# Kernel optimization log

Measured on AMD Instinct MI355X. Metric: run time of the kernel, lower is better.

The kernel has to match this reference:

```python
import jax, jax.numpy as jnp
import numpy as np
from jax import lax

B, C, T = 8, 512, 2048
TEMP = 0.07
EPS = 1e-12


def setup_inputs() -> dict:
    key = jax.random.key(0)
    k1, k2, k3, k4 = jax.random.split(key, 4)
    x = jax.random.normal(k1, (B, C, T), dtype=jnp.float32)
    w_qkv = jax.random.normal(k2, (3 * C, C, 1), dtype=jnp.float32) * (1.0 / np.sqrt(C))
    w_dw = jax.random.normal(k3, (3 * C, 1, 3), dtype=jnp.float32) * (1.0 / np.sqrt(3))
    w_proj = jax.random.normal(k4, (C, C, 1), dtype=jnp.float32) * (1.0 / np.sqrt(C))
    return {"x": x, "w_qkv": w_qkv, "w_dw": w_dw, "w_proj": w_proj}


def _l2norm_ch(a):
    # F.normalize(a, dim=1): divide by L2 norm over channel dim, clamped at eps
    n = jnp.sqrt(jnp.sum(a * a, axis=1, keepdims=True))
    return a / jnp.maximum(n, EPS)


def reference(x, w_qkv, w_dw, w_proj):
    # 1x1 conv: [B,C,T] x [3C,C] -> [B,3C,T]
    qkv = jnp.einsum('bct,oc->bot', x, w_qkv[:, :, 0])
    # depthwise conv, kernel 3, padding 1, groups = 3C
    qkv = lax.conv_general_dilated(
        qkv, w_dw, window_strides=(1,), padding=[(1, 1)],
        dimension_numbers=('NCH', 'OIH', 'NCH'), feature_group_count=3 * C)
    q, k, v = jnp.split(qkv, 3, axis=1)  # each [B,C,T]
    q = _l2norm_ch(q)
    k = _l2norm_ch(k)
    # attn over tokens: [B,T,T]
    attn = jax.nn.softmax(jnp.einsum('bct,bcs->bts', q, k) / TEMP, axis=-1)
    out = jnp.einsum('bts,bcs->bct', attn, v)  # [B,C,T]
    return jnp.einsum('bct,oc->bot', out, w_proj[:, :, 0])
```

## Files before the change

kernel.cpp:

```cpp
#include <hip/hip_runtime.h>
#include <math.h>

static constexpr int B_ = 8, C_ = 512, T_ = 2048, C3_ = 1536;
static constexpr float INV_TEMP = 1.0f / 0.07f;

typedef __attribute__((ext_vector_type(8))) short short8;
typedef __attribute__((ext_vector_type(4))) float floatx4;

__device__ __forceinline__ float b2f(unsigned short u) {
  union { unsigned int i; float f; } v; v.i = ((unsigned int)u) << 16; return v.f;
}
__device__ __forceinline__ unsigned short f2b(float f) {
  union { float f; unsigned int i; } v; v.f = f;
  const unsigned int x = v.i;
  return (unsigned short)((x + 0x7FFFu + ((x >> 16) & 1u)) >> 16);
}
__device__ __forceinline__ void gld16(const unsigned short* g, unsigned short* l) {
  __builtin_amdgcn_global_load_lds(
      (const __attribute__((address_space(1))) void*)g,
      (__attribute__((address_space(3))) void*)l, 16, 0, 0);
}

template<bool OUT_BF16, int MODE>
__global__ __launch_bounds__(256)
void gemm_tn(const unsigned short* __restrict__ A, const unsigned short* __restrict__ B,
             void* __restrict__ Cout, int K, int lda, int ldb, int ldc,
             long long sA, long long sB, long long sC,
             const float* __restrict__ rs, const float* __restrict__ cs,
             float* __restrict__ denom, int rcStride, float scale)
{
  constexpr int NL = 4;

  const int bz = blockIdx.z;
  A += (long long)bz * sA;
  B += (long long)bz * sB;
  if (MODE == 2) { rs += (long long)bz * rcStride; cs += (long long)bz * rcStride;
                   denom += (long long)bz * rcStride; }
  if (MODE == 3) { rs += (long long)bz * rcStride; }
  const int m0 = blockIdx.y * 128, n0 = blockIdx.x * 128;
  const int tid = threadIdx.x;
  const int w = tid >> 6, lane = tid & 63;
  const int wm = (w >> 1) * 64, wn = (w & 1) * 64;
  const int rl = lane & 15, qd = lane >> 4;

  __shared__ __align__(16) unsigned short As[3][128 * 32];
  __shared__ __align__(16) unsigned short Bs[3][128 * 32];

  const int sr = lane >> 2, sg = lane & 3;
  const int ml0 = 32 * w + sr, ml1 = ml0 + 16;
  const int q0 = sg ^ ((ml0 >> 1) & 3), q1 = sg ^ ((ml1 >> 1) & 3);
  const unsigned short* gA0 = A + (long long)(m0 + ml0) * lda + q0 * 8;
  const unsigned short* gA1 = A + (long long)(m0 + ml1) * lda + q1 * 8;
  const unsigned short* gB0 = B + (long long)(n0 + ml0) * ldb + q0 * 8;
  const unsigned short* gB1 = B + (long long)(n0 + ml1) * ldb + q1 * 8;

  int aoff[4], boff[4];
  #pragma unroll
  for (int i = 0; i < 4; ++i) {
    const int mr = wm + i * 16 + rl;
    aoff[i] = mr * 32 + ((qd ^ ((mr >> 1) & 3)) * 8);
    const int nr = wn + i * 16 + rl;
    boff[i] = nr * 32 + ((qd ^ ((nr >> 1) & 3)) * 8);
  }

  floatx4 acc[4][4];
  #pragma unroll
  for (int i = 0; i < 4; ++i)
    #pragma unroll
    for (int j = 0; j < 4; ++j) acc[i][j] = 0.0f;

  auto stage = [&](int t, int bf) {
    const int ko = t * 32;
    gld16(gA0 + ko, As[bf] + (32 * w) * 32);
    gld16(gA1 + ko, As[bf] + (32 * w + 16) * 32);
    gld16(gB0 + ko, Bs[bf] + (32 * w) * 32);
    gld16(gB1 + ko, Bs[bf] + (32 * w + 16) * 32);
  };
  auto compute = [&](int bf) {
    short8 fa[4], fb[4];
    #pragma unroll
    for (int i = 0; i < 4; ++i) fa[i] = *(const short8*)(As[bf] + aoff[i]);
    #pragma unroll
    for (int j = 0; j < 4; ++j) fb[j] = *(const short8*)(Bs[bf] + boff[j]);
    #pragma unroll
    for (int i = 0; i < 4; ++i)
      #pragma unroll
      for (int j = 0; j < 4; ++j)
        acc[i][j] = __builtin_amdgcn_mfma_f32_16x16x32_bf16(fa[i], fb[j], acc[i][j], 0, 0, 0);
  };

  const int niter = K >> 5;
  stage(0, 0);
  stage(1, 1);
  int buf = 0;
  for (int i = 0; i < niter - 1; ++i) {
    asm volatile("s_waitcnt vmcnt(%0)\n\ts_barrier" :: "i"(NL) : "memory");
    if (i + 2 < niter) {
      int nb = buf + 2; if (nb >= 3) nb -= 3;
      stage(i + 2, nb);
    }
    compute(buf);
    if (++buf == 3) buf = 0;
  }
  asm volatile("s_waitcnt vmcnt(0)\n\ts_barrier" ::: "memory");
  compute(buf);

  #pragma unroll
  for (int i = 0; i < 4; ++i) {
    #pragma unroll
    for (int r = 0; r < 4; ++r) {
      const int row = m0 + wm + i * 16 + qd * 4 + r;
      float rowf = 0.f;
      if (MODE == 2) rowf = rs[row] * scale;
      if (MODE == 3) rowf = 1.0f / rs[row];
      float rsum = 0.f;
      #pragma unroll
      for (int j = 0; j < 4; ++j) {
        const int col = n0 + wn + j * 16 + rl;
        float v = acc[i][j][r];
        if (MODE == 2) {
          const float s = v * rowf * cs[col];
          const unsigned short pb = f2b(__expf(s - scale));
          rsum += b2f(pb);
          ((unsigned short*)Cout)[(long long)bz * sC + (long long)row * ldc + col] = pb;
          continue;
        }
        if (MODE == 3) v *= rowf;
        const long long idx = (long long)bz * sC + (long long)row * ldc + col;
        if (OUT_BF16) ((unsigned short*)Cout)[idx] = f2b(v);
        else          ((float*)Cout)[idx] = v;
      }
      if (MODE == 2) {
        #pragma unroll
        for (int m = 1; m < 16; m <<= 1) rsum += __shfl_xor(rsum, m);
        if (rl == 0) atomicAdd(denom + row, rsum);
      }
    }
  }
}

__global__ __launch_bounds__(256)
void zero_f(float* __restrict__ p, int n)
{
  const int i = blockIdx.x * 256 + threadIdx.x;
  if (i < n) p[i] = 0.f;
}

__global__ __launch_bounds__(256)
void conv_xT(const float* __restrict__ x, unsigned short* __restrict__ xT)
{
  const int b = blockIdx.z, t0 = blockIdx.x * 32, c0 = blockIdx.y * 32;
  const int tx = threadIdx.x & 31, ty = threadIdx.x >> 5;
  __shared__ float tile[32][33];
  const float* src = x + (long long)b * C_ * T_;
  #pragma unroll
  for (int r = 0; r < 4; ++r)
    tile[ty + 8 * r][tx] = src[(long long)(c0 + ty + 8 * r) * T_ + t0 + tx];
  __syncthreads();
  unsigned short* dst = xT + (long long)b * T_ * C_;
  #pragma unroll
  for (int r = 0; r < 4; ++r)
    dst[(long long)(t0 + ty + 8 * r) * C_ + c0 + tx] = f2b(tile[tx][ty + 8 * r]);
}

__global__ __launch_bounds__(256)
void conv_bf(const float* __restrict__ in, unsigned short* __restrict__ out, int n)
{
  const int i = blockIdx.x * 256 + threadIdx.x;
  if (i < n) out[i] = f2b(in[i]);
}

__global__ __launch_bounds__(256)
void dw_v(const unsigned short* __restrict__ qkv, const float* __restrict__ wdw,
          unsigned short* __restrict__ vout)
{
  const long long idx = (long long)blockIdx.x * 256 + threadIdx.x;
  const int t = (int)(idx % T_);
  const long long rem = idx / T_;
  const int c = (int)(rem % C_), b = (int)(rem / C_);
  const unsigned short* src = qkv + ((long long)(b * C3_ + 2 * C_ + c)) * T_;
  const float* wp = wdw + (2 * C_ + c) * 3;
  const float xm = (t > 0)      ? b2f(src[t - 1]) : 0.f;
  const float x0 = b2f(src[t]);
  const float xp = (t < T_ - 1) ? b2f(src[t + 1]) : 0.f;
  vout[(long long)(b * C_ + c) * T_ + t] = f2b(fmaf(wp[0], xm, fmaf(wp[1], x0, wp[2] * xp)));
}

__global__ __launch_bounds__(256)
void dw_qk_t(const unsigned short* __restrict__ qkv, const float* __restrict__ wdw,
             unsigned short* __restrict__ qT, unsigned short* __restrict__ kT)
{
  const int bz = blockIdx.z, b = bz >> 1, p = bz & 1;
  const int t0 = blockIdx.x * 32, c0 = blockIdx.y * 32;
  const int tx = threadIdx.x & 31, ty = threadIdx.x >> 5;
  __shared__ float tin[32][34];
  __shared__ float tout[32][33];
  const int chb = b * C3_ + p * C_;
  #pragma unroll
  for (int r = 0; r < 4; ++r) {
    const int cy = ty + 8 * r;
    const unsigned short* src = qkv + (long long)(chb + c0 + cy) * T_;
    int t = t0 - 1 + tx;
    tin[cy][tx] = (t >= 0 && t < T_) ? b2f(src[t]) : 0.f;
    if (tx < 2) {
      const int t2 = t0 + 31 + tx;
      tin[cy][32 + tx] = (t2 < T_) ? b2f(src[t2]) : 0.f;
    }
  }
  __syncthreads();
  #pragma unroll
  for (int r = 0; r < 4; ++r) {
    const int cy = ty + 8 * r;
    const float* wp = wdw + (long long)(p * C_ + c0 + cy) * 3;
    tout[tx][cy] = fmaf(wp[0], tin[cy][tx], fmaf(wp[1], tin[cy][tx + 1], wp[2] * tin[cy][tx + 2]));
  }
  __syncthreads();
  unsigned short* dst = (p == 0 ? qT : kT) + (long long)b * T_ * C_;
  #pragma unroll
  for (int r = 0; r < 4; ++r)
    dst[(long long)(t0 + ty + 8 * r) * C_ + c0 + tx] = f2b(tout[ty + 8 * r][tx]);
}

__global__ __launch_bounds__(256)
void norms_k(const unsigned short* __restrict__ qT, const unsigned short* __restrict__ kT,
             float* __restrict__ inv_nq, float* __restrict__ inv_nk)
{
  const int wave = threadIdx.x >> 6, lane = threadIdx.x & 63;
  const long long row = (long long)blockIdx.x * 4 + wave;
  const unsigned short* src = (blockIdx.y == 0 ? qT : kT) + row * C_ + lane * 8;
  const uint4 u = *(const uint4*)src;
  float ss = 0.f;
  const unsigned int uu[4] = {u.x, u.y, u.z, u.w};
  #pragma unroll
  for (int i = 0; i < 4; ++i) {
    const float lo = b2f(uu[i] & 0xFFFF), hi = b2f(uu[i] >> 16);
    ss = fmaf(lo, lo, ss); ss = fmaf(hi, hi, ss);
  }
  #pragma unroll
  for (int m = 32; m; m >>= 1) ss += __shfl_xor(ss, m);
  if (lane == 0)
    (blockIdx.y == 0 ? inv_nq : inv_nk)[row] = 1.f / fmaxf(sqrtf(ss), 1e-12f);
}

extern "C" void kernel_launch(void* const* d_in, const int* in_sizes, int n_in,
                              void* d_out, int out_size, void* d_ws, size_t ws_size,
                              hipStream_t stream)
{
  const float* x      = (const float*)d_in[0];
  const float* w_qkv  = (const float*)d_in[1];
  const float* w_dw   = (const float*)d_in[2];
  const float* w_proj = (const float*)d_in[3];
  float* out = (float*)d_out;

  char* base = (char*)d_ws;
  unsigned short* xT      = (unsigned short*)base;
  unsigned short* wqkv_bf = (unsigned short*)(base + 16777216);
  unsigned short* av_t    = (unsigned short*)base;
  char* p = base + 67108864;
  unsigned short* qT = (unsigned short*)p; p += 16777216;
  unsigned short* kT = (unsigned short*)p; p += 16777216;
  unsigned short* vb = (unsigned short*)p; p += 16777216;
  unsigned short* attn   = (unsigned short*)p;
  unsigned short* qkv_bf = (unsigned short*)p;
  p += 67108864;
  unsigned short* wproj_bf = (unsigned short*)p; p += 524288;
  float* inv_nq = (float*)p; p += 65536;
  float* inv_nk = (float*)p; p += 65536;
  float* denom  = (float*)p;

  const long long TC = (long long)T_ * C_, TT = (long long)T_ * T_;

  conv_xT<<<dim3(T_ / 32, C_ / 32, B_), 256, 0, stream>>>(x, xT);
  conv_bf<<<(C3_ * C_) / 256, 256, 0, stream>>>(w_qkv, wqkv_bf, C3_ * C_);
  conv_bf<<<(C_ * C_) / 256, 256, 0, stream>>>(w_proj, wproj_bf, C_ * C_);
  zero_f<<<(B_ * T_) / 256, 256, 0, stream>>>(denom, B_ * T_);

  gemm_tn<true, 0><<<dim3(16, 12, B_), 256, 0, stream>>>(
      wqkv_bf, xT, qkv_bf, C_, C_, C_, T_,
      0LL, TC, (long long)C3_ * T_, nullptr, nullptr, nullptr, 0, 1.f);

  dw_v<<<(int)(((long long)B_ * C_ * T_) / 256), 256, 0, stream>>>(qkv_bf, w_dw, vb);
  dw_qk_t<<<dim3(T_ / 32, C_ / 32, B_ * 2), 256, 0, stream>>>(qkv_bf, w_dw, qT, kT);

  norms_k<<<dim3((B_ * T_) / 4, 2), 256, 0, stream>>>(qT, kT, inv_nq, inv_nk);

  gemm_tn<true, 2><<<dim3(16, 16, B_), 256, 0, stream>>>(
      qT, kT, attn, C_, C_, C_, T_,
      TC, TC, TT, inv_nq, inv_nk, denom, T_, INV_TEMP);

  gemm_tn<true, 3><<<dim3(4, 16, B_), 256, 0, stream>>>(
      attn, vb, av_t, T_, T_, T_, C_,
      TT, (long long)C_ * T_, TC, denom, nullptr, nullptr, T_, 1.f);

  gemm_tn<false, 0><<<dim3(16, 4, B_), 256, 0, stream>>>(
      wproj_bf, av_t, out, C_, C_, C_, T_,
      0LL, TC, (long long)C_ * T_, nullptr, nullptr, nullptr, 0, 1.f);
}
```

Before: 335.3 us.

## Replace 128x128 GEMM with 256x256 eight-wave ping-pong pipelined kernel

Rewrites the shared GEMM kernel to use 256x256 output tiles with 512 threads, K-step 64, and 128KB of dynamic LDS. A fine-grained schedule of barriers and s_setprio interleaves LDS fragment reads, async global-to-LDS loads and MFMA blocks. The aim is more data reuse per tile and more overlap of loads with compute. The trade-offs are fewer blocks for the small GEMMs (for example 128 blocks for the AV and projection GEMMs), heavy LDS use and many barriers.

```diff
diff --git a/kernel.cpp b/kernel.cpp
--- a/kernel.cpp
+++ b/kernel.cpp
@@ -21,15 +21,21 @@
       (__attribute__((address_space(3))) void*)l, 16, 0, 0);
 }
 
+#define FENCE  asm volatile("" ::: "memory")
+#define BAR()  do { FENCE; __builtin_amdgcn_s_barrier(); FENCE; } while (0)
+#define LGKM0  asm volatile("s_waitcnt lgkmcnt(0)" ::: "memory")
+#define VMC4   asm volatile("s_waitcnt vmcnt(4)" ::: "memory")
+#define VMC0   asm volatile("s_waitcnt vmcnt(0)" ::: "memory")
+
 template<bool OUT_BF16, int MODE>
-__global__ __launch_bounds__(256)
-void gemm_tn(const unsigned short* __restrict__ A, const unsigned short* __restrict__ B,
+__global__ __launch_bounds__(512, 2)
+void gemm256(const unsigned short* __restrict__ A, const unsigned short* __restrict__ B,
              void* __restrict__ Cout, int K, int lda, int ldb, int ldc,
              long long sA, long long sB, long long sC,
              const float* __restrict__ rs, const float* __restrict__ cs,
              float* __restrict__ denom, int rcStride, float scale)
 {
-  constexpr int NL = 4;
+  extern __shared__ unsigned short S[];
 
   const int bz = blockIdx.z;
   A += (long long)bz * sA;
@@ -37,76 +43,125 @@
   if (MODE == 2) { rs += (long long)bz * rcStride; cs += (long long)bz * rcStride;
                    denom += (long long)bz * rcStride; }
   if (MODE == 3) { rs += (long long)bz * rcStride; }
-  const int m0 = blockIdx.y * 128, n0 = blockIdx.x * 128;
+  const int m0 = blockIdx.y * 256, n0 = blockIdx.x * 256;
   const int tid = threadIdx.x;
   const int w = tid >> 6, lane = tid & 63;
-  const int wm = (w >> 1) * 64, wn = (w & 1) * 64;
   const int rl = lane & 15, qd = lane >> 4;
-
-  __shared__ __align__(16) unsigned short As[3][128 * 32];
-  __shared__ __align__(16) unsigned short Bs[3][128 * 32];
-
-  const int sr = lane >> 2, sg = lane & 3;
-  const int ml0 = 32 * w + sr, ml1 = ml0 + 16;
-  const int q0 = sg ^ ((ml0 >> 1) & 3), q1 = sg ^ ((ml1 >> 1) & 3);
-  const unsigned short* gA0 = A + (long long)(m0 + ml0) * lda + q0 * 8;
-  const unsigned short* gA1 = A + (long long)(m0 + ml1) * lda + q1 * 8;
-  const unsigned short* gB0 = B + (long long)(n0 + ml0) * ldb + q0 * 8;
-  const unsigned short* gB1 = B + (long long)(n0 + ml1) * ldb + q1 * 8;
-
-  int aoff[4], boff[4];
-  #pragma unroll
-  for (int i = 0; i < 4; ++i) {
-    const int mr = wm + i * 16 + rl;
-    aoff[i] = mr * 32 + ((qd ^ ((mr >> 1) & 3)) * 8);
-    const int nr = wn + i * 16 + rl;
-    boff[i] = nr * 32 + ((qd ^ ((nr >> 1) & 3)) * 8);
-  }
-
-  floatx4 acc[4][4];
-  #pragma unroll
-  for (int i = 0; i < 4; ++i)
+  const int wm = (w >> 2) * 128, wn = (w & 3) * 64;
+
+  const int lr = lane >> 3;
+  const int lg = ((lane & 7) ^ lr) * 8;
+  const unsigned short* gA = A + (long long)(m0 + w * 8 + lr) * lda + lg;
+  const unsigned short* gB = B + (long long)(n0 + w * 8 + lr) * ldb + lg;
+
+  const int g0 = (qd ^ (rl & 7)) * 8;
+  const int g1 = ((4 + qd) ^ (rl & 7)) * 8;
+  const int aBase = (wm + rl) * 64, bBase = (wn + rl) * 64;
+
+  floatx4 acc[8][4];
+  #pragma unroll
+  for (int i = 0; i < 8; ++i)
     #pragma unroll
     for (int j = 0; j < 4; ++j) acc[i][j] = 0.0f;
 
-  auto stage = [&](int t, int bf) {
-    const int ko = t * 32;
-    gld16(gA0 + ko, As[bf] + (32 * w) * 32);
-    gld16(gA1 + ko, As[bf] + (32 * w + 16) * 32);
-    gld16(gB0 + ko, Bs[bf] + (32 * w) * 32);
-    gld16(gB1 + ko, Bs[bf] + (32 * w + 16) * 32);
-  };
-  auto compute = [&](int bf) {
-    short8 fa[4], fb[4];
-    #pragma unroll
-    for (int i = 0; i < 4; ++i) fa[i] = *(const short8*)(As[bf] + aoff[i]);
-    #pragma unroll
-    for (int j = 0; j < 4; ++j) fb[j] = *(const short8*)(Bs[bf] + boff[j]);
+  auto stA = [&](int buf, int h, int kt) {
+    unsigned short* d = S + buf * 32768 + h * 8192 + w * 512;
+    const unsigned short* s = gA + (long long)(h * 128) * lda + kt * 64;
+    gld16(s, d);
+    gld16(s + (long long)64 * lda, d + 4096);
+  };
+  auto stB = [&](int buf, int h, int kt) {
+    unsigned short* d = S + buf * 32768 + 16384 + h * 8192 + w * 512;
+    const unsigned short* s = gB + (long long)(h * 128) * ldb + kt * 64;
+    gld16(s, d);
+    gld16(s + (long long)64 * ldb, d + 4096);
+  };
+
+  short8 fa[4][2], fl[2][2], fr[2][2];
+  auto rdA = [&](int buf, int ih) {
+    const unsigned short* p = S + buf * 32768 + aBase + ih * 4096;
+    #pragma unroll
+    for (int i = 0; i < 4; ++i) {
+      fa[i][0] = *(const short8*)(p + i * 1024 + g0);
+      fa[i][1] = *(const short8*)(p + i * 1024 + g1);
+    }
+  };
+  auto rdB = [&](short8 (&fb)[2][2], int buf, int jh) {
+    const unsigned short* p = S + buf * 32768 + 16384 + bBase + jh * 2048;
+    #pragma unroll
+    for (int j = 0; j < 2; ++j) {
+      fb[j][0] = *(const short8*)(p + j * 1024 + g0);
+      fb[j][1] = *(const short8*)(p + j * 1024 + g1);
+    }
+  };
+  auto mm = [&](short8 (&fb)[2][2], int ih, int jh) {
     #pragma unroll
     for (int i = 0; i < 4; ++i)
       #pragma unroll
-      for (int j = 0; j < 4; ++j)
-        acc[i][j] = __builtin_amdgcn_mfma_f32_16x16x32_bf16(fa[i], fb[j], acc[i][j], 0, 0, 0);
-  };
-
-  const int niter = K >> 5;
-  stage(0, 0);
-  stage(1, 1);
-  int buf = 0;
-  for (int i = 0; i < niter - 1; ++i) {
-    asm volatile("s_waitcnt vmcnt(%0)\n\ts_barrier" :: "i"(NL) : "memory");
-    if (i + 2 < niter) {
-      int nb = buf + 2; if (nb >= 3) nb -= 3;
-      stage(i + 2, nb);
-    }
-    compute(buf);
-    if (++buf == 3) buf = 0;
-  }
-  asm volatile("s_waitcnt vmcnt(0)\n\ts_barrier" ::: "memory");
-  compute(buf);
-
-  #pragma unroll
-  for (int i = 0; i < 4; ++i) {
+      for (int j = 0; j < 2; ++j) {
+        floatx4& a = acc[ih * 4 + i][jh * 2 + j];
+        a = __builtin_amdgcn_mfma_f32_16x16x32_bf16(fa[i][0], fb[j][0], a, 0, 0, 0);
+        a = __builtin_amdgcn_mfma_f32_16x16x32_bf16(fa[i][1], fb[j][1], a, 0, 0, 0);
+      }
+  };
+
+  auto iter = [&](int kt, bool st2, bool st3, bool tail) {
+    rdA(0, 0); rdB(fl, 0, 0);
+    stA(1, 0, kt + 1);
+    BAR(); LGKM0;
+    __builtin_amdgcn_s_setprio(1); mm(fl, 0, 0); __builtin_amdgcn_s_setprio(0);
+    BAR();
+    rdB(fr, 0, 1);
+    stA(1, 1, kt + 1);
+    BAR(); LGKM0;
+    __builtin_amdgcn_s_setprio(1); mm(fr, 0, 1); __builtin_amdgcn_s_setprio(0);
+    BAR();
+    rdA(0, 1);
+    if (st2) stB(0, 0, kt + 2);
+    BAR(); LGKM0;
+    __builtin_amdgcn_s_setprio(1); mm(fl, 1, 0); __builtin_amdgcn_s_setprio(0);
+    BAR();
+    if (st2) stB(0, 1, kt + 2);
+    if (tail) { VMC0; } else { VMC4; }
+    BAR();
+    __builtin_amdgcn_s_setprio(1); mm(fr, 1, 1); __builtin_amdgcn_s_setprio(0);
+    BAR();
+    rdA(1, 0); rdB(fl, 1, 0);
+    if (st2) stA(0, 0, kt + 2);
+    BAR(); LGKM0;
+    __builtin_amdgcn_s_setprio(1); mm(fl, 0, 0); __builtin_amdgcn_s_setprio(0);
+    BAR();
+    rdB(fr, 1, 1);
+    if (st2) stA(0, 1, kt + 2);
+    BAR(); LGKM0;
+    __builtin_amdgcn_s_setprio(1); mm(fr, 0, 1); __builtin_amdgcn_s_setprio(0);
+    BAR();
+    rdA(1, 1);
+    if (st3) stB(1, 0, kt + 3);
+    BAR(); LGKM0;
+    __builtin_amdgcn_s_setprio(1); mm(fl, 1, 0); __builtin_amdgcn_s_setprio(0);
+    BAR();
+    if (st3) stB(1, 1, kt + 3);
+    if (!tail) { VMC4; }
+    BAR();
+    __builtin_amdgcn_s_setprio(1); mm(fr, 1, 1); __builtin_amdgcn_s_setprio(0);
+    BAR();
+  };
+
+  const int niter = K >> 7;
+  stB(0, 0, 0); stB(0, 1, 0); stA(0, 0, 0); stA(0, 1, 0);
+  stB(1, 0, 1); stB(1, 1, 1);
+  VMC4; BAR();
+  for (int i = 0; i < niter - 1; ++i) iter(2 * i, true, true, false);
+  iter(2 * (niter - 1), false, false, true);
+
+  float cf4[4];
+  if (MODE == 2) {
+    #pragma unroll
+    for (int j = 0; j < 4; ++j) cf4[j] = cs[n0 + wn + j * 16 + rl];
+  }
+  #pragma unroll
+  for (int i = 0; i < 8; ++i) {
     #pragma unroll
     for (int r = 0; r < 4; ++r) {
       const int row = m0 + wm + i * 16 + qd * 4 + r;
@@ -119,7 +174,7 @@
         const int col = n0 + wn + j * 16 + rl;
         float v = acc[i][j][r];
         if (MODE == 2) {
-          const float s = v * rowf * cs[col];
+          const float s = v * rowf * cf4[j];
           const unsigned short pb = f2b(__expf(s - scale));
           rsum += b2f(pb);
           ((unsigned short*)Cout)[(long long)bz * sC + (long long)row * ldc + col] = pb;
@@ -252,6 +307,19 @@
   const float* w_proj = (const float*)d_in[3];
   float* out = (float*)d_out;
 
+  static int attr_done = 0;
+  if (!attr_done) {
+    hipFuncSetAttribute((const void*)&gemm256<true, 0>,
+                        hipFuncAttributeMaxDynamicSharedMemorySize, 131072);
+    hipFuncSetAttribute((const void*)&gemm256<true, 2>,
+                        hipFuncAttributeMaxDynamicSharedMemorySize, 131072);
+    hipFuncSetAttribute((const void*)&gemm256<true, 3>,
+                        hipFuncAttributeMaxDynamicSharedMemorySize, 131072);
+    hipFuncSetAttribute((const void*)&gemm256<false, 0>,
+                        hipFuncAttributeMaxDynamicSharedMemorySize, 131072);
+    attr_done = 1;
+  }
+
   char* base = (char*)d_ws;
   unsigned short* xT      = (unsigned short*)base;
   unsigned short* wqkv_bf = (unsigned short*)(base + 16777216);
@@ -275,7 +343,7 @@
   conv_bf<<<(C_ * C_) / 256, 256, 0, stream>>>(w_proj, wproj_bf, C_ * C_);
   zero_f<<<(B_ * T_) / 256, 256, 0, stream>>>(denom, B_ * T_);
 
-  gemm_tn<true, 0><<<dim3(16, 12, B_), 256, 0, stream>>>(
+  gemm256<true, 0><<<dim3(8, 6, B_), 512, 131072, stream>>>(
       wqkv_bf, xT, qkv_bf, C_, C_, C_, T_,
       0LL, TC, (long long)C3_ * T_, nullptr, nullptr, nullptr, 0, 1.f);
 
@@ -284,15 +352,15 @@
 
   norms_k<<<dim3((B_ * T_) / 4, 2), 256, 0, stream>>>(qT, kT, inv_nq, inv_nk);
 
-  gemm_tn<true, 2><<<dim3(16, 16, B_), 256, 0, stream>>>(
+  gemm256<true, 2><<<dim3(8, 8, B_), 512, 131072, stream>>>(
       qT, kT, attn, C_, C_, C_, T_,
       TC, TC, TT, inv_nq, inv_nk, denom, T_, INV_TEMP);
 
-  gemm_tn<true, 3><<<dim3(4, 16, B_), 256, 0, stream>>>(
+  gemm256<true, 3><<<dim3(2, 8, B_), 512, 131072, stream>>>(
       attn, vb, av_t, T_, T_, T_, C_,
       TT, (long long)C_ * T_, TC, denom, nullptr, nullptr, T_, 1.f);
 
-  gemm_tn<false, 0><<<dim3(16, 4, B_), 256, 0, stream>>>(
+  gemm256<false, 0><<<dim3(8, 2, B_), 512, 131072, stream>>>(
       wproj_bf, av_t, out, C_, C_, C_, T_,
       0LL, TC, (long long)C_ * T_, nullptr, nullptr, nullptr, 0, 1.f);
 }
```

New measurement: 340.9 us. No clear change (+1.7%).

## Fuse depthwise conv with norms and use 256x256-tile QK GEMM

Applied to the files above, without the earlier changes.

Merges the v and q/k depthwise-conv kernels into one launch. The sum-of-squares norm reduction moves into the conv epilogue through atomics, followed by a small finalize kernel, which removes the separate norms pass that re-read qT/kT. The QK^T softmax-numerator GEMM is switched to a new 1024-thread kernel with 256x256 tiles and triple-buffered dynamic LDS, to raise data reuse. The risks are lower occupancy from the 96KB LDS blocks, the cost of the atomic contention, and only 512 blocks to spread across the CUs.

```diff
diff --git a/kernel.cpp b/kernel.cpp
--- a/kernel.cpp
+++ b/kernel.cpp
@@ -139,11 +139,125 @@
   }
 }
 
+template<bool OUT_BF16, int MODE>
+__global__ __launch_bounds__(1024)
+void gemm_tn1024(const unsigned short* __restrict__ A, const unsigned short* __restrict__ B,
+                 void* __restrict__ Cout, int K, int lda, int ldb, int ldc,
+                 long long sA, long long sB, long long sC,
+                 const float* __restrict__ rs, const float* __restrict__ cs,
+                 float* __restrict__ denom, int rcStride, float scale)
+{
+  extern __shared__ unsigned short S[];
+
+  const int bz = blockIdx.z;
+  A += (long long)bz * sA;
+  B += (long long)bz * sB;
+  if (MODE == 2) { rs += (long long)bz * rcStride; cs += (long long)bz * rcStride;
+                   denom += (long long)bz * rcStride; }
+  if (MODE == 3) { rs += (long long)bz * rcStride; }
+  const int m0 = blockIdx.y * 256, n0 = blockIdx.x * 256;
+  const int tid = threadIdx.x;
+  const int w = tid >> 6, lane = tid & 63;
+  const int wm = (w >> 2) * 64, wn = (w & 3) * 64;
+  const int rl = lane & 15, qd = lane >> 4;
+
+  const int srow = w * 16 + (lane >> 2), sg = lane & 3;
+  const int qa = sg ^ ((srow >> 1) & 3);
+  const unsigned short* gA = A + (long long)(m0 + srow) * lda + qa * 8;
+  const unsigned short* gB = B + (long long)(n0 + srow) * ldb + qa * 8;
+
+  const int ar = wm + rl, br = wn + rl;
+  const int aoff0 = ar * 32 + ((qd ^ ((ar >> 1) & 3)) * 8);
+  const int boff0 = br * 32 + ((qd ^ ((br >> 1) & 3)) * 8);
+
+  floatx4 acc[4][4];
+  #pragma unroll
+  for (int i = 0; i < 4; ++i)
+    #pragma unroll
+    for (int j = 0; j < 4; ++j) acc[i][j] = 0.0f;
+
+  auto stage = [&](int t, int bf) {
+    const int ko = t * 32;
+    gld16(gA + ko, S + bf * 16384 + w * 512);
+    gld16(gB + ko, S + bf * 16384 + 8192 + w * 512);
+  };
+  auto compute = [&](int bf) {
+    short8 fa[4], fb[4];
+    const unsigned short* pA = S + bf * 16384 + aoff0;
+    const unsigned short* pB = S + bf * 16384 + 8192 + boff0;
+    #pragma unroll
+    for (int i = 0; i < 4; ++i) fa[i] = *(const short8*)(pA + i * 512);
+    #pragma unroll
+    for (int j = 0; j < 4; ++j) fb[j] = *(const short8*)(pB + j * 512);
+    #pragma unroll
+    for (int i = 0; i < 4; ++i)
+      #pragma unroll
+      for (int j = 0; j < 4; ++j)
+        acc[i][j] = __builtin_amdgcn_mfma_f32_16x16x32_bf16(fa[i], fb[j], acc[i][j], 0, 0, 0);
+  };
+
+  const int niter = K >> 5;
+  stage(0, 0);
+  stage(1, 1);
+  int buf = 0;
+  for (int i = 0; i < niter - 1; ++i) {
+    asm volatile("s_waitcnt vmcnt(2)\n\ts_barrier" ::: "memory");
+    if (i + 2 < niter) {
+      int nb = buf + 2; if (nb >= 3) nb -= 3;
+      stage(i + 2, nb);
+    }
+    compute(buf);
+    if (++buf == 3) buf = 0;
+  }
+  asm volatile("s_waitcnt vmcnt(0)\n\ts_barrier" ::: "memory");
+  compute(buf);
+
+  #pragma unroll
+  for (int i = 0; i < 4; ++i) {
+    #pragma unroll
+    for (int r = 0; r < 4; ++r) {
+      const int row = m0 + wm + i * 16 + qd * 4 + r;
+      float rowf = 0.f;
+      if (MODE == 2) rowf = rs[row] * scale;
+      if (MODE == 3) rowf = 1.0f / rs[row];
+      float rsum = 0.f;
+      #pragma unroll
+      for (int j = 0; j < 4; ++j) {
+        const int col = n0 + wn + j * 16 + rl;
+        float v = acc[i][j][r];
+        if (MODE == 2) {
+          const float s = v * rowf * cs[col];
+          const unsigned short pb = f2b(__expf(s - scale));
+          rsum += b2f(pb);
+          ((unsigned short*)Cout)[(long long)bz * sC + (long long)row * ldc + col] = pb;
+          continue;
+        }
+        if (MODE == 3) v *= rowf;
+        const long long idx = (long long)bz * sC + (long long)row * ldc + col;
+        if (OUT_BF16) ((unsigned short*)Cout)[idx] = f2b(v);
+        else          ((float*)Cout)[idx] = v;
+      }
+      if (MODE == 2) {
+        #pragma unroll
+        for (int m = 1; m < 16; m <<= 1) rsum += __shfl_xor(rsum, m);
+        if (rl == 0) atomicAdd(denom + row, rsum);
+      }
+    }
+  }
+}
+
 __global__ __launch_bounds__(256)
 void zero_f(float* __restrict__ p, int n)
 {
   const int i = blockIdx.x * 256 + threadIdx.x;
   if (i < n) p[i] = 0.f;
+}
+
+__global__ __launch_bounds__(256)
+void fin_inv(float* __restrict__ p, int n)
+{
+  const int i = blockIdx.x * 256 + threadIdx.x;
+  if (i < n) p[i] = 1.f / fmaxf(sqrtf(p[i]), 1e-12f);
 }
 
 __global__ __launch_bounds__(256)
@@ -171,26 +285,12 @@
 }
 
 __global__ __launch_bounds__(256)
-void dw_v(const unsigned short* __restrict__ qkv, const float* __restrict__ wdw,
-          unsigned short* __restrict__ vout)
-{
-  const long long idx = (long long)blockIdx.x * 256 + threadIdx.x;
-  const int t = (int)(idx % T_);
-  const long long rem = idx / T_;
-  const int c = (int)(rem % C_), b = (int)(rem / C_);
-  const unsigned short* src = qkv + ((long long)(b * C3_ + 2 * C_ + c)) * T_;
-  const float* wp = wdw + (2 * C_ + c) * 3;
-  const float xm = (t > 0)      ? b2f(src[t - 1]) : 0.f;
-  const float x0 = b2f(src[t]);
-  const float xp = (t < T_ - 1) ? b2f(src[t + 1]) : 0.f;
-  vout[(long long)(b * C_ + c) * T_ + t] = f2b(fmaf(wp[0], xm, fmaf(wp[1], x0, wp[2] * xp)));
-}
-
-__global__ __launch_bounds__(256)
-void dw_qk_t(const unsigned short* __restrict__ qkv, const float* __restrict__ wdw,
-             unsigned short* __restrict__ qT, unsigned short* __restrict__ kT)
-{
-  const int bz = blockIdx.z, b = bz >> 1, p = bz & 1;
+void dw_qkv_t(const unsigned short* __restrict__ qkv, const float* __restrict__ wdw,
+              unsigned short* __restrict__ qT, unsigned short* __restrict__ kT,
+              unsigned short* __restrict__ vout,
+              float* __restrict__ sq_q, float* __restrict__ sq_k)
+{
+  const int bz = blockIdx.z, b = bz / 3, p = bz % 3;
   const int t0 = blockIdx.x * 32, c0 = blockIdx.y * 32;
   const int tx = threadIdx.x & 31, ty = threadIdx.x >> 5;
   __shared__ float tin[32][34];
@@ -208,38 +308,36 @@
     }
   }
   __syncthreads();
+  if (p == 2) {
+    #pragma unroll
+    for (int r = 0; r < 4; ++r) {
+      const int cy = ty + 8 * r;
+      const float* wp = wdw + (2 * C_ + c0 + cy) * 3;
+      const float v = fmaf(wp[0], tin[cy][tx], fmaf(wp[1], tin[cy][tx + 1], wp[2] * tin[cy][tx + 2]));
+      vout[(long long)(b * C_ + c0 + cy) * T_ + t0 + tx] = f2b(v);
+    }
+    return;
+  }
   #pragma unroll
   for (int r = 0; r < 4; ++r) {
     const int cy = ty + 8 * r;
-    const float* wp = wdw + (long long)(p * C_ + c0 + cy) * 3;
+    const float* wp = wdw + (p * C_ + c0 + cy) * 3;
     tout[tx][cy] = fmaf(wp[0], tin[cy][tx], fmaf(wp[1], tin[cy][tx + 1], wp[2] * tin[cy][tx + 2]));
   }
   __syncthreads();
   unsigned short* dst = (p == 0 ? qT : kT) + (long long)b * T_ * C_;
-  #pragma unroll
-  for (int r = 0; r < 4; ++r)
-    dst[(long long)(t0 + ty + 8 * r) * C_ + c0 + tx] = f2b(tout[ty + 8 * r][tx]);
-}
-
-__global__ __launch_bounds__(256)
-void norms_k(const unsigned short* __restrict__ qT, const unsigned short* __restrict__ kT,
-             float* __restrict__ inv_nq, float* __restrict__ inv_nk)
-{
-  const int wave = threadIdx.x >> 6, lane = threadIdx.x & 63;
-  const long long row = (long long)blockIdx.x * 4 + wave;
-  const unsigned short* src = (blockIdx.y == 0 ? qT : kT) + row * C_ + lane * 8;
-  const uint4 u = *(const uint4*)src;
-  float ss = 0.f;
-  const unsigned int uu[4] = {u.x, u.y, u.z, u.w};
-  #pragma unroll
-  for (int i = 0; i < 4; ++i) {
-    const float lo = b2f(uu[i] & 0xFFFF), hi = b2f(uu[i] >> 16);
-    ss = fmaf(lo, lo, ss); ss = fmaf(hi, hi, ss);
-  }
-  #pragma unroll
-  for (int m = 32; m; m >>= 1) ss += __shfl_xor(ss, m);
-  if (lane == 0)
-    (blockIdx.y == 0 ? inv_nq : inv_nk)[row] = 1.f / fmaxf(sqrtf(ss), 1e-12f);
+  float* sq = (p == 0 ? sq_q : sq_k) + (long long)b * T_;
+  #pragma unroll
+  for (int r = 0; r < 4; ++r) {
+    const int tl = ty + 8 * r;
+    const unsigned short ub = f2b(tout[tl][tx]);
+    dst[(long long)(t0 + tl) * C_ + c0 + tx] = ub;
+    const float fv = b2f(ub);
+    float ssq = fv * fv;
+    #pragma unroll
+    for (int m = 1; m < 32; m <<= 1) ssq += __shfl_xor(ssq, m);
+    if (tx == 0) atomicAdd(sq + t0 + tl, ssq);
+  }
 }
 
 extern "C" void kernel_launch(void* const* d_in, const int* in_sizes, int n_in,
@@ -251,6 +349,13 @@
   const float* w_dw   = (const float*)d_in[2];
   const float* w_proj = (const float*)d_in[3];
   float* out = (float*)d_out;
+
+  static int attr_done = 0;
+  if (!attr_done) {
+    hipFuncSetAttribute((const void*)&gemm_tn1024<true, 2>,
+                        hipFuncAttributeMaxDynamicSharedMemorySize, 98304);
+    attr_done = 1;
+  }
 
   char* base = (char*)d_ws;
   unsigned short* xT      = (unsigned short*)base;
@@ -273,18 +378,17 @@
   conv_xT<<<dim3(T_ / 32, C_ / 32, B_), 256, 0, stream>>>(x, xT);
   conv_bf<<<(C3_ * C_) / 256, 256, 0, stream>>>(w_qkv, wqkv_bf, C3_ * C_);
   conv_bf<<<(C_ * C_) / 256, 256, 0, stream>>>(w_proj, wproj_bf, C_ * C_);
-  zero_f<<<(B_ * T_) / 256, 256, 0, stream>>>(denom, B_ * T_);
+  zero_f<<<(3 * B_ * T_) / 256, 256, 0, stream>>>(inv_nq, 3 * B_ * T_);
 
   gemm_tn<true, 0><<<dim3(16, 12, B_), 256, 0, stream>>>(
       wqkv_bf, xT, qkv_bf, C_, C_, C_, T_,
       0LL, TC, (long long)C3_ * T_, nullptr, nullptr, nullptr, 0, 1.f);
 
-  dw_v<<<(int)(((long long)B_ * C_ * T_) / 256), 256, 0, stream>>>(qkv_bf, w_dw, vb);
-  dw_qk_t<<<dim3(T_ / 32, C_ / 32, B_ * 2), 256, 0, stream>>>(qkv_bf, w_dw, qT, kT);
-
-  norms_k<<<dim3((B_ * T_) / 4, 2), 256, 0, stream>>>(qT, kT, inv_nq, inv_nk);
-
-  gemm_tn<true, 2><<<dim3(16, 16, B_), 256, 0, stream>>>(
+  dw_qkv_t<<<dim3(T_ / 32, C_ / 32, B_ * 3), 256, 0, stream>>>(
+      qkv_bf, w_dw, qT, kT, vb, inv_nq, inv_nk);
+  fin_inv<<<(2 * B_ * T_) / 256, 256, 0, stream>>>(inv_nq, 2 * B_ * T_);
+
+  gemm_tn1024<true, 2><<<dim3(8, 8, B_), 1024, 98304, stream>>>(
       qT, kT, attn, C_, C_, C_, T_,
       TC, TC, TT, inv_nq, inv_nk, denom, T_, INV_TEMP);
 
```

Result: no change. 332.7 us (-0.8%).
